# Performance work log

Hardware: AMD Instinct MI355X
Metric: run time of the kernel (lower is better)

Reference implementation:

```python
import jax, jax.numpy as jnp
import numpy as np
from jax import lax

K_NEIGHBORS = 3  # n_neighbors


def _divide_no_nan(x, d):
    # tf.math.divide_no_nan semantics: 0 where denominator is 0
    safe = jnp.where(d == 0, 1.0, d)
    return jnp.where(d == 0, 0.0, x / safe)


def setup_inputs() -> dict:
    key = jax.random.key(0)
    k1, k2, k3 = jax.random.split(key, 3)
    B, N, D, C = 512, 200000, 27, 10
    queries = jax.random.normal(k1, (B, D), dtype=jnp.float32)
    features = jax.random.normal(k2, (N, D), dtype=jnp.float32)
    cls = jax.random.randint(k3, (N,), 0, C)
    labels = jax.nn.one_hot(cls, C, dtype=jnp.float32)
    return {"queries": queries, "features": features, "labels": labels}


def reference(queries, features, labels):
    # scale_tensor: per-dim max of |training features| (computed at init in the TF model)
    scale = jnp.max(jnp.abs(features), axis=0)              # (D,)
    fs = _divide_no_nan(features, scale)                    # (N, D)
    qs = _divide_no_nan(queries, scale)                     # (B, D)

    # pairwise Euclidean distances (B, N) == tf.norm(fs - q, axis=1) per query
    d2 = (jnp.sum(fs * fs, axis=1)[None, :]
          - 2.0 * qs @ fs.T
          + jnp.sum(qs * qs, axis=1)[:, None])
    dist = jnp.sqrt(jnp.maximum(d2, 0.0))                   # (B, N)

    neg_kd, idx = lax.top_k(-dist, K_NEIGHBORS)             # (B, K)
    kd = -neg_kd                                            # k smallest distances
    lab = labels[idx]                                       # (B, K, C) gather

    # weighted vote: sum_k label_k / dist_k, then argmax -> one-hot
    safe_kd = jnp.where(kd == 0, 1.0, kd)
    weighted = jnp.sum(lab / safe_kd[..., None], axis=1)    # (B, C)
    vote = jax.nn.one_hot(jnp.argmax(weighted, axis=-1), labels.shape[1],
                          dtype=labels.dtype)

    # exact-match branch: if min distance == 0, take nearest neighbor's label
    zero_hit = (jnp.min(kd, axis=1, keepdims=True) == 0)    # (B, 1)
    result = jnp.where(zero_hit, lab[:, 0, :], vote)        # (B, C)

    # concatenated (k_smallest_distances, result_tensor) per query: (B, K + C)
    return jnp.concatenate([kd, result], axis=-1)
```

## Files before the change

### kernel.cpp

```cpp
#include <hip/hip_runtime.h>
#include <math.h>

#define NQ     512
#define DD     27
#define NC     10
#define KK     3
#define NTHR   256
#define NSLICE 256
#define NBLK   (NSLICE*4)
#define NCAND  (NSLICE*3)

static __device__ __forceinline__ unsigned fbits(float x){ return __float_as_uint(x); }

__global__ void k_scale(const float* __restrict__ feats, unsigned* __restrict__ scale_bits,
                        int total, int total_f4) {
  __shared__ unsigned smax[DD];
  int t = threadIdx.x;
  if (t < DD) smax[t] = 0u;
  __syncthreads();
  int gid = blockIdx.x * blockDim.x + t;
  int stride = gridDim.x * blockDim.x;
  const float4* f4 = (const float4*)feats;
  float m0=0.f, m1=0.f, m2=0.f, m3=0.f;
  for (int i = gid; i < total_f4; i += stride) {
    float4 v = f4[i];
    m0 = fmaxf(m0, fabsf(v.x));
    m1 = fmaxf(m1, fabsf(v.y));
    m2 = fmaxf(m2, fabsf(v.z));
    m3 = fmaxf(m3, fabsf(v.w));
  }
  int d0 = (4*gid) % DD;
  atomicMax(&smax[d0],          fbits(m0));
  atomicMax(&smax[(d0+1)%DD],   fbits(m1));
  atomicMax(&smax[(d0+2)%DD],   fbits(m2));
  atomicMax(&smax[(d0+3)%DD],   fbits(m3));
  if (gid == 0) {
    for (int i = total_f4*4; i < total; ++i)
      atomicMax(&scale_bits[i % DD], fbits(fabsf(feats[i])));
  }
  __syncthreads();
  if (t < DD) atomicMax(&scale_bits[t], smax[t]);
}

__global__ void k_prepfn(const float* __restrict__ queries, const float* __restrict__ feats,
                         const unsigned* __restrict__ scale_bits, float* __restrict__ qp,
                         float* __restrict__ qnorm, float* __restrict__ fnorm2, int nfeat) {
  __shared__ float rs[DD];
  int t = threadIdx.x;
  if (t < DD) {
    float s = __uint_as_float(scale_bits[t]);
    rs[t] = (s == 0.f) ? 0.f : 1.f / s;
  }
  __syncthreads();
  int f = blockIdx.x * blockDim.x + t;
  if (f < nfeat) {
    const float* row = feats + (size_t)f*DD;
    float acc = 0.f;
    #pragma unroll
    for (int d = 0; d < DD; ++d) { float v = row[d] * rs[d]; acc = fmaf(v, v, acc); }
    fnorm2[f] = acc;
  }
  if (blockIdx.x == 0) {
    for (int qq = t; qq < NQ; qq += NTHR) {
      float nrm = 0.f;
      #pragma unroll
      for (int d = 0; d < DD; ++d) {
        float v = queries[qq*DD + d] * rs[d];
        qp[qq*DD + d] = v * rs[d];
        nrm = fmaf(v, v, nrm);
      }
      qnorm[qq] = nrm;
    }
  }
}

#define TINS(acc, fi, sA, sB, sC, iA, iB, iC) do {                        \
    if ((acc) > sC) {                                                     \
      if ((acc) > sA)      { sC=sB;iC=iB; sB=sA;iB=iA; sA=(acc);iA=(fi); }\
      else if ((acc) > sB) { sC=sB;iC=iB; sB=(acc);iB=(fi); }             \
      else                 { sC=(acc); iC=(fi); }                         \
    }                                                                     \
  } while (0)

#define DECLQ(d)  float q0_##d = qp[qa*DD + (d)]; float q1_##d = qp[(qa+64)*DD + (d)];
#define QF(d)     { float fv_ = row[d]; a0 = fmaf(fv_, q0_##d, a0); a1 = fmaf(fv_, q1_##d, a1); }

__global__ __launch_bounds__(NTHR)
__attribute__((amdgpu_waves_per_eu(4, 4)))
void k_knn(
    const float* __restrict__ feats, const float* __restrict__ qp,
    const float* __restrict__ fnorm2, float* __restrict__ pd2v,
    int* __restrict__ pd2i, int nfeat) {
  int t = threadIdx.x;
  int lane = t & 63;
  int w = __builtin_amdgcn_readfirstlane(t >> 6);
  int b = blockIdx.x;
  int qt    = b >> 8;
  int slice = b & (NSLICE-1);

  int qa = qt*128 + lane;
  DECLQ(0)  DECLQ(1)  DECLQ(2)  DECLQ(3)  DECLQ(4)  DECLQ(5)  DECLQ(6)
  DECLQ(7)  DECLQ(8)  DECLQ(9)  DECLQ(10) DECLQ(11) DECLQ(12) DECLQ(13)
  DECLQ(14) DECLQ(15) DECLQ(16) DECLQ(17) DECLQ(18) DECLQ(19) DECLQ(20)
  DECLQ(21) DECLQ(22) DECLQ(23) DECLQ(24) DECLQ(25) DECLQ(26)
  asm volatile("" : "+v"(q0_0),"+v"(q0_1),"+v"(q0_2),"+v"(q0_3),"+v"(q0_4),
                    "+v"(q0_5),"+v"(q0_6),"+v"(q0_7),"+v"(q0_8),"+v"(q0_9),
                    "+v"(q0_10),"+v"(q0_11),"+v"(q0_12),"+v"(q0_13));
  asm volatile("" : "+v"(q0_14),"+v"(q0_15),"+v"(q0_16),"+v"(q0_17),"+v"(q0_18),
                    "+v"(q0_19),"+v"(q0_20),"+v"(q0_21),"+v"(q0_22),"+v"(q0_23),
                    "+v"(q0_24),"+v"(q0_25),"+v"(q0_26));
  asm volatile("" : "+v"(q1_0),"+v"(q1_1),"+v"(q1_2),"+v"(q1_3),"+v"(q1_4),
                    "+v"(q1_5),"+v"(q1_6),"+v"(q1_7),"+v"(q1_8),"+v"(q1_9),
                    "+v"(q1_10),"+v"(q1_11),"+v"(q1_12),"+v"(q1_13));
  asm volatile("" : "+v"(q1_14),"+v"(q1_15),"+v"(q1_16),"+v"(q1_17),"+v"(q1_18),
                    "+v"(q1_19),"+v"(q1_20),"+v"(q1_21),"+v"(q1_22),"+v"(q1_23),
                    "+v"(q1_24),"+v"(q1_25),"+v"(q1_26));

  float s00=-INFINITY, s01=-INFINITY, s02=-INFINITY;
  float s10=-INFINITY, s11=-INFINITY, s12=-INFINITY;
  int   i00=0x7fffffff, i01=0x7fffffff, i02=0x7fffffff;
  int   i10=0x7fffffff, i11=0x7fffffff, i12=0x7fffffff;

  int S = (nfeat + NSLICE - 1) / NSLICE;
  int base = slice * S;
  int cnt = nfeat - base; if (cnt > S) cnt = S; if (cnt < 0) cnt = 0;
  int fb = base + (cnt * w) / 4;
  int fe = base + (cnt * (w+1)) / 4;

  #pragma unroll 2
  for (int f = fb; f < fe; ++f) {
    const float* row = feats + (size_t)f * DD;
    float fn = fnorm2[f];
    float a0 = -0.5f * fn;
    float a1 = -0.5f * fn;
    QF(0)  QF(1)  QF(2)  QF(3)  QF(4)  QF(5)  QF(6)  QF(7)  QF(8)
    QF(9)  QF(10) QF(11) QF(12) QF(13) QF(14) QF(15) QF(16) QF(17)
    QF(18) QF(19) QF(20) QF(21) QF(22) QF(23) QF(24) QF(25) QF(26)
    TINS(a0, f, s00, s01, s02, i00, i01, i02);
    TINS(a1, f, s10, s11, s12, i10, i11, i12);
  }

  __shared__ float sv[4][128][3];
  __shared__ int   sx[4][128][3];
  sv[w][lane][0]    = s00; sv[w][lane][1]    = s01; sv[w][lane][2]    = s02;
  sx[w][lane][0]    = i00; sx[w][lane][1]    = i01; sx[w][lane][2]    = i02;
  sv[w][lane+64][0] = s10; sv[w][lane+64][1] = s11; sv[w][lane+64][2] = s12;
  sx[w][lane+64][0] = i10; sx[w][lane+64][1] = i11; sx[w][lane+64][2] = i12;
  __syncthreads();
  if (t < 128) {
    float b0=-INFINITY, b1=-INFINITY, b2=-INFINITY;
    int   x0=0x7fffffff, x1=0x7fffffff, x2=0x7fffffff;
    #pragma unroll
    for (int ww = 0; ww < 4; ++ww) {
      #pragma unroll
      for (int j = 0; j < 3; ++j) {
        float v = sv[ww][t][j]; int ix = sx[ww][t][j];
        if (v > b2 || (v == b2 && ix < x2)) {
          if (v > b0 || (v == b0 && ix < x0))      { b2=b1;x2=x1; b1=b0;x1=x0; b0=v;x0=ix; }
          else if (v > b1 || (v == b1 && ix < x1)) { b2=b1;x2=x1; b1=v;x1=ix; }
          else                                     { b2=v; x2=ix; }
        }
      }
    }
    int q = qt*128 + t;
    long o = (long)q * NCAND + slice*3;
    pd2v[o+0] = -2.f*b0; pd2v[o+1] = -2.f*b1; pd2v[o+2] = -2.f*b2;
    pd2i[o+0] = x0;      pd2i[o+1] = x1;      pd2i[o+2] = x2;
  }
}

#define INS(vv, ii) do { \
  if ((vv) < c2 || ((vv) == c2 && (ii) < j2)) { \
    if ((vv) < c0 || ((vv) == c0 && (ii) < j0))      { c2=c1;j2=j1; c1=c0;j1=j0; c0=(vv);j0=(ii); } \
    else if ((vv) < c1 || ((vv) == c1 && (ii) < j1)) { c2=c1;j2=j1; c1=(vv);j1=(ii); } \
    else                                             { c2=(vv); j2=(ii); } \
  } \
} while (0)

__global__ __launch_bounds__(NTHR) void k_merge(
    const float* __restrict__ pd2v, const int* __restrict__ pd2i,
    const float* __restrict__ qnorm, const float* __restrict__ labels,
    float* __restrict__ out) {
  __shared__ float sk[NTHR*3];
  __shared__ int   si[NTHR*3];
  int q = blockIdx.x, t = threadIdx.x;
  float c0=INFINITY, c1=INFINITY, c2=INFINITY;
  int   j0=0x7fffffff, j1=0x7fffffff, j2=0x7fffffff;
  const float* pv = pd2v + (long)q * NCAND;
  const int*   pi = pd2i + (long)q * NCAND;
  for (int i = t; i < NCAND; i += NTHR) {
    float v = pv[i]; int ix = pi[i];
    INS(v, ix);
  }
  sk[t*3+0]=c0; sk[t*3+1]=c1; sk[t*3+2]=c2;
  si[t*3+0]=j0; si[t*3+1]=j1; si[t*3+2]=j2;
  __syncthreads();
  if (t < 64) {
    for (int s = 1; s < 4; ++s) {
      int bb = t + s*64;
      #pragma unroll
      for (int k = 0; k < 3; ++k) { float v = sk[bb*3+k]; int ix = si[bb*3+k]; INS(v, ix); }
    }
    sk[t*3+0]=c0; sk[t*3+1]=c1; sk[t*3+2]=c2;
    si[t*3+0]=j0; si[t*3+1]=j1; si[t*3+2]=j2;
  }
  __syncthreads();
  if (t == 0) {
    for (int s = 1; s < 64; ++s) {
      #pragma unroll
      for (int k = 0; k < 3; ++k) { float v = sk[s*3+k]; int ix = si[s*3+k]; INS(v, ix); }
    }
    float qn = qnorm[q];
    float kd0 = sqrtf(fmaxf(c0 + qn, 0.f));
    float kd1 = sqrtf(fmaxf(c1 + qn, 0.f));
    float kd2 = sqrtf(fmaxf(c2 + qn, 0.f));
    const float* l0 = labels + (long)j0 * NC;
    const float* l1 = labels + (long)j1 * NC;
    const float* l2 = labels + (long)j2 * NC;
    float inv0 = 1.f / ((kd0 == 0.f) ? 1.f : kd0);
    float inv1 = 1.f / ((kd1 == 0.f) ? 1.f : kd1);
    float inv2 = 1.f / ((kd2 == 0.f) ? 1.f : kd2);
    float wv[NC];
    #pragma unroll
    for (int cc = 0; cc < NC; ++cc)
      wv[cc] = l0[cc]*inv0 + l1[cc]*inv1 + l2[cc]*inv2;
    int am = 0; float bw = wv[0];
    #pragma unroll
    for (int cc = 1; cc < NC; ++cc) if (wv[cc] > bw) { bw = wv[cc]; am = cc; }
    float* o = out + q * (KK + NC);
    o[0] = kd0; o[1] = kd1; o[2] = kd2;
    if (kd0 == 0.f) {
      #pragma unroll
      for (int cc = 0; cc < NC; ++cc) o[3+cc] = l0[cc];
    } else {
      #pragma unroll
      for (int cc = 0; cc < NC; ++cc) o[3+cc] = (cc == am) ? 1.f : 0.f;
    }
  }
}

extern "C" void kernel_launch(void* const* d_in, const int* in_sizes, int n_in,
                              void* d_out, int out_size, void* d_ws, size_t ws_size,
                              hipStream_t stream) {
  const float* queries = (const float*)d_in[0];
  const float* feats   = (const float*)d_in[1];
  const float* labels  = (const float*)d_in[2];
  float* out = (float*)d_out;
  char*  ws  = (char*)d_ws;

  int total = in_sizes[1];
  int nfeat = total / DD;

  unsigned* scale_bits = (unsigned*)ws;
  float* qnorm  = (float*)(ws + 512);
  float* qp     = (float*)(ws + 4096);
  float* fnorm2 = (float*)(ws + 65536);
  float* pd2v   = (float*)(ws + 1048576);
  int*   pd2i   = (int*)(ws + 1048576 + 2097152);

  hipMemsetAsync(ws, 0, 128, stream);
  k_scale<<<864, 256, 0, stream>>>(feats, scale_bits, total, total / 4);
  k_prepfn<<<(nfeat + 255) / 256, 256, 0, stream>>>(queries, feats, scale_bits,
                                                    qp, qnorm, fnorm2, nfeat);
  k_knn  <<<NBLK, NTHR, 0, stream>>>(feats, qp, fnorm2, pd2v, pd2i, nfeat);
  k_merge<<<NQ, NTHR, 0, stream>>>(pd2v, pd2i, qnorm, labels, out);
}
```

Before: 257.5 us.

## Prescale features into padded 28-float rows with folded norm, float4 KNN loads

The prep kernel now writes scaled features into a padded 28-wide buffer whose last element holds -0.5*norm, staging rows through shared memory for coalesced reads. Queries are padded the same way with a trailing 1.0, so the distance score becomes a plain 28-term dot product loaded as seven float4s. The KNN kernel now handles one query per thread instead of two, doubling the block count to 2048. This removes unaligned scalar row loads and the separate norm fetch, at the cost of writing and re-reading an extra 22 MB padded copy and reusing each feature load across half as many queries.

```diff
diff --git a/kernel.cpp b/kernel.cpp
--- a/kernel.cpp
+++ b/kernel.cpp
@@ -3,11 +3,13 @@
 
 #define NQ     512
 #define DD     27
+#define DP     28
 #define NC     10
 #define KK     3
 #define NTHR   256
 #define NSLICE 256
-#define NBLK   (NSLICE*4)
+#define NGRP   8
+#define NBLK   (NSLICE*NGRP)
 #define NCAND  (NSLICE*3)
 
 static __device__ __forceinline__ unsigned fbits(float x){ return __float_as_uint(x); }
@@ -42,23 +44,39 @@
   if (t < DD) atomicMax(&scale_bits[t], smax[t]);
 }
 
-__global__ void k_prepfn(const float* __restrict__ queries, const float* __restrict__ feats,
-                         const unsigned* __restrict__ scale_bits, float* __restrict__ qp,
-                         float* __restrict__ qnorm, float* __restrict__ fnorm2, int nfeat) {
+__global__ __launch_bounds__(NTHR) void k_prepfn(
+    const float* __restrict__ queries, const float* __restrict__ feats,
+    const unsigned* __restrict__ scale_bits, float* __restrict__ qp,
+    float* __restrict__ qnorm, float* __restrict__ pf, int nfeat) {
   __shared__ float rs[DD];
+  __shared__ float rows[NTHR*DD];
   int t = threadIdx.x;
   if (t < DD) {
     float s = __uint_as_float(scale_bits[t]);
     rs[t] = (s == 0.f) ? 0.f : 1.f / s;
   }
   __syncthreads();
-  int f = blockIdx.x * blockDim.x + t;
+  int fbase = blockIdx.x * NTHR;
+  int gbase = fbase * DD;
+  int ntot  = nfeat * DD;
+  #pragma unroll
+  for (int j = 0; j < DD; ++j) {
+    int idx = t + j*NTHR;
+    int g = gbase + idx;
+    rows[idx] = (g < ntot) ? feats[g] : 0.f;
+  }
+  __syncthreads();
+  int f = fbase + t;
   if (f < nfeat) {
-    const float* row = feats + (size_t)f*DD;
+    float* dst = pf + (size_t)f * DP;
     float acc = 0.f;
     #pragma unroll
-    for (int d = 0; d < DD; ++d) { float v = row[d] * rs[d]; acc = fmaf(v, v, acc); }
-    fnorm2[f] = acc;
+    for (int d = 0; d < DD; ++d) {
+      float x = rows[t*DD + d] * rs[d];
+      dst[d] = x;
+      acc = fmaf(x, x, acc);
+    }
+    dst[DD] = -0.5f * acc;
   }
   if (blockIdx.x == 0) {
     for (int qq = t; qq < NQ; qq += NTHR) {
@@ -66,60 +84,47 @@
       #pragma unroll
       for (int d = 0; d < DD; ++d) {
         float v = queries[qq*DD + d] * rs[d];
-        qp[qq*DD + d] = v * rs[d];
+        qp[qq*DP + d] = v;
         nrm = fmaf(v, v, nrm);
       }
+      qp[qq*DP + DD] = 1.0f;
       qnorm[qq] = nrm;
     }
   }
 }
 
-#define TINS(acc, fi, sA, sB, sC, iA, iB, iC) do {                        \
-    if ((acc) > sC) {                                                     \
-      if ((acc) > sA)      { sC=sB;iC=iB; sB=sA;iB=iA; sA=(acc);iA=(fi); }\
-      else if ((acc) > sB) { sC=sB;iC=iB; sB=(acc);iB=(fi); }             \
-      else                 { sC=(acc); iC=(fi); }                         \
+#define TINS(acc, fi) do {                                                \
+    if ((acc) > s2) {                                                     \
+      if ((acc) > s0)      { s2=s1;i2=i1; s1=s0;i1=i0; s0=(acc);i0=(fi); }\
+      else if ((acc) > s1) { s2=s1;i2=i1; s1=(acc);i1=(fi); }             \
+      else                 { s2=(acc); i2=(fi); }                         \
     }                                                                     \
   } while (0)
 
-#define DECLQ(d)  float q0_##d = qp[qa*DD + (d)]; float q1_##d = qp[(qa+64)*DD + (d)];
-#define QF(d)     { float fv_ = row[d]; a0 = fmaf(fv_, q0_##d, a0); a1 = fmaf(fv_, q1_##d, a1); }
-
-__global__ __launch_bounds__(NTHR)
-__attribute__((amdgpu_waves_per_eu(4, 4)))
-void k_knn(
-    const float* __restrict__ feats, const float* __restrict__ qp,
-    const float* __restrict__ fnorm2, float* __restrict__ pd2v,
-    int* __restrict__ pd2i, int nfeat) {
+#define FDOT(rv, qv) do {                    \
+    a = fmaf((rv).x, (qv).x, a);             \
+    a = fmaf((rv).y, (qv).y, a);             \
+    a = fmaf((rv).z, (qv).z, a);             \
+    a = fmaf((rv).w, (qv).w, a);             \
+  } while (0)
+
+__global__ __launch_bounds__(NTHR) void k_knn(
+    const float4* __restrict__ pf4, const float4* __restrict__ qp4,
+    float* __restrict__ pd2v, int* __restrict__ pd2i, int nfeat) {
   int t = threadIdx.x;
   int lane = t & 63;
-  int w = __builtin_amdgcn_readfirstlane(t >> 6);
+  int w = t >> 6;
   int b = blockIdx.x;
-  int qt    = b >> 8;
+  int qg    = b >> 8;
   int slice = b & (NSLICE-1);
 
-  int qa = qt*128 + lane;
-  DECLQ(0)  DECLQ(1)  DECLQ(2)  DECLQ(3)  DECLQ(4)  DECLQ(5)  DECLQ(6)
-  DECLQ(7)  DECLQ(8)  DECLQ(9)  DECLQ(10) DECLQ(11) DECLQ(12) DECLQ(13)
-  DECLQ(14) DECLQ(15) DECLQ(16) DECLQ(17) DECLQ(18) DECLQ(19) DECLQ(20)
-  DECLQ(21) DECLQ(22) DECLQ(23) DECLQ(24) DECLQ(25) DECLQ(26)
-  asm volatile("" : "+v"(q0_0),"+v"(q0_1),"+v"(q0_2),"+v"(q0_3),"+v"(q0_4),
-                    "+v"(q0_5),"+v"(q0_6),"+v"(q0_7),"+v"(q0_8),"+v"(q0_9),
-                    "+v"(q0_10),"+v"(q0_11),"+v"(q0_12),"+v"(q0_13));
-  asm volatile("" : "+v"(q0_14),"+v"(q0_15),"+v"(q0_16),"+v"(q0_17),"+v"(q0_18),
-                    "+v"(q0_19),"+v"(q0_20),"+v"(q0_21),"+v"(q0_22),"+v"(q0_23),
-                    "+v"(q0_24),"+v"(q0_25),"+v"(q0_26));
-  asm volatile("" : "+v"(q1_0),"+v"(q1_1),"+v"(q1_2),"+v"(q1_3),"+v"(q1_4),
-                    "+v"(q1_5),"+v"(q1_6),"+v"(q1_7),"+v"(q1_8),"+v"(q1_9),
-                    "+v"(q1_10),"+v"(q1_11),"+v"(q1_12),"+v"(q1_13));
-  asm volatile("" : "+v"(q1_14),"+v"(q1_15),"+v"(q1_16),"+v"(q1_17),"+v"(q1_18),
-                    "+v"(q1_19),"+v"(q1_20),"+v"(q1_21),"+v"(q1_22),"+v"(q1_23),
-                    "+v"(q1_24),"+v"(q1_25),"+v"(q1_26));
-
-  float s00=-INFINITY, s01=-INFINITY, s02=-INFINITY;
-  float s10=-INFINITY, s11=-INFINITY, s12=-INFINITY;
-  int   i00=0x7fffffff, i01=0x7fffffff, i02=0x7fffffff;
-  int   i10=0x7fffffff, i11=0x7fffffff, i12=0x7fffffff;
+  int myq = qg*64 + lane;
+  const float4* qb = qp4 + (size_t)myq * 7;
+  float4 q0 = qb[0], q1 = qb[1], q2 = qb[2], q3 = qb[3],
+         q4 = qb[4], q5 = qb[5], q6 = qb[6];
+
+  float s0=-INFINITY, s1=-INFINITY, s2=-INFINITY;
+  int   i0=0x7fffffff, i1=0x7fffffff, i2=0x7fffffff;
 
   int S = (nfeat + NSLICE - 1) / NSLICE;
   int base = slice * S;
@@ -127,27 +132,22 @@
   int fb = base + (cnt * w) / 4;
   int fe = base + (cnt * (w+1)) / 4;
 
-  #pragma unroll 2
   for (int f = fb; f < fe; ++f) {
-    const float* row = feats + (size_t)f * DD;
-    float fn = fnorm2[f];
-    float a0 = -0.5f * fn;
-    float a1 = -0.5f * fn;
-    QF(0)  QF(1)  QF(2)  QF(3)  QF(4)  QF(5)  QF(6)  QF(7)  QF(8)
-    QF(9)  QF(10) QF(11) QF(12) QF(13) QF(14) QF(15) QF(16) QF(17)
-    QF(18) QF(19) QF(20) QF(21) QF(22) QF(23) QF(24) QF(25) QF(26)
-    TINS(a0, f, s00, s01, s02, i00, i01, i02);
-    TINS(a1, f, s10, s11, s12, i10, i11, i12);
-  }
-
-  __shared__ float sv[4][128][3];
-  __shared__ int   sx[4][128][3];
-  sv[w][lane][0]    = s00; sv[w][lane][1]    = s01; sv[w][lane][2]    = s02;
-  sx[w][lane][0]    = i00; sx[w][lane][1]    = i01; sx[w][lane][2]    = i02;
-  sv[w][lane+64][0] = s10; sv[w][lane+64][1] = s11; sv[w][lane+64][2] = s12;
-  sx[w][lane+64][0] = i10; sx[w][lane+64][1] = i11; sx[w][lane+64][2] = i12;
-  __syncthreads();
-  if (t < 128) {
+    const float4* r = pf4 + (size_t)f * 7;
+    float4 r0 = r[0], r1 = r[1], r2 = r[2], r3 = r[3],
+           r4 = r[4], r5 = r[5], r6 = r[6];
+    float a = 0.f;
+    FDOT(r0, q0); FDOT(r1, q1); FDOT(r2, q2); FDOT(r3, q3);
+    FDOT(r4, q4); FDOT(r5, q5); FDOT(r6, q6);
+    TINS(a, f);
+  }
+
+  __shared__ float sv[4][64][3];
+  __shared__ int   sx[4][64][3];
+  sv[w][lane][0] = s0; sv[w][lane][1] = s1; sv[w][lane][2] = s2;
+  sx[w][lane][0] = i0; sx[w][lane][1] = i1; sx[w][lane][2] = i2;
+  __syncthreads();
+  if (t < 64) {
     float b0=-INFINITY, b1=-INFINITY, b2=-INFINITY;
     int   x0=0x7fffffff, x1=0x7fffffff, x2=0x7fffffff;
     #pragma unroll
@@ -162,7 +162,7 @@
         }
       }
     }
-    int q = qt*128 + t;
+    int q = qg*64 + t;
     long o = (long)q * NCAND + slice*3;
     pd2v[o+0] = -2.f*b0; pd2v[o+1] = -2.f*b1; pd2v[o+2] = -2.f*b2;
     pd2i[o+0] = x0;      pd2i[o+1] = x1;      pd2i[o+2] = x2;
@@ -254,14 +254,14 @@
   unsigned* scale_bits = (unsigned*)ws;
   float* qnorm  = (float*)(ws + 512);
   float* qp     = (float*)(ws + 4096);
-  float* fnorm2 = (float*)(ws + 65536);
-  float* pd2v   = (float*)(ws + 1048576);
-  int*   pd2i   = (int*)(ws + 1048576 + 2097152);
+  float* pd2v   = (float*)(ws + 65536);
+  int*   pd2i   = (int*)(ws + 65536 + 1572864);
+  float* pf     = (float*)(ws + 4194304);
 
   hipMemsetAsync(ws, 0, 128, stream);
   k_scale<<<864, 256, 0, stream>>>(feats, scale_bits, total, total / 4);
-  k_prepfn<<<(nfeat + 255) / 256, 256, 0, stream>>>(queries, feats, scale_bits,
-                                                    qp, qnorm, fnorm2, nfeat);
-  k_knn  <<<NBLK, NTHR, 0, stream>>>(feats, qp, fnorm2, pd2v, pd2i, nfeat);
+  k_prepfn<<<(nfeat + NTHR - 1) / NTHR, NTHR, 0, stream>>>(queries, feats, scale_bits,
+                                                           qp, qnorm, pf, nfeat);
+  k_knn  <<<NBLK, NTHR, 0, stream>>>((const float4*)pf, (const float4*)qp, pd2v, pd2i, nfeat);
   k_merge<<<NQ, NTHR, 0, stream>>>(pd2v, pd2i, qnorm, labels, out);
 }
```

Result: slower. 433.8 us (+68.5%).
